# Performance work log

Measured on AMD Instinct MI355X. Metric: run time of the kernel, lower is better.

The kernel has to match this reference:

```python
import jax, jax.numpy as jnp
import numpy as np

S = 2048
D = 2048
H = 16
HD = D // H
N_CHARS = 1024
LN_EPS = 1e-5


def setup_inputs() -> dict:
    key = jax.random.key(0)
    ks = jax.random.split(key, 12)
    byte_repr = jax.random.normal(ks[0], (S, D), dtype=jnp.float32)
    categories = jax.random.randint(ks[1], (S,), 0, 32, dtype=jnp.int32)
    case = jax.random.randint(ks[2], (S,), 0, 3, dtype=jnp.int32)
    combining = jax.random.randint(ks[3], (S,), 0, 2, dtype=jnp.int32)
    seg_ids = jnp.sort(jax.random.randint(ks[4], (S,), 0, N_CHARS, dtype=jnp.int32))
    sc = 0.02
    cat_emb = jax.random.normal(ks[5], (32, D), dtype=jnp.float32) * sc
    case_emb = jax.random.normal(ks[6], (3, D), dtype=jnp.float32) * sc
    comb_emb = jax.random.normal(ks[7], (2, D), dtype=jnp.float32) * sc
    ln_g = jnp.ones((D,), dtype=jnp.float32)
    ln_b = jnp.zeros((D,), dtype=jnp.float32)
    in_w = jax.random.normal(ks[8], (3 * D, D), dtype=jnp.float32) * (1.0 / np.sqrt(D))
    in_b = jnp.zeros((3 * D,), dtype=jnp.float32)
    out_w = jax.random.normal(ks[9], (D, D), dtype=jnp.float32) * (1.0 / np.sqrt(D))
    out_b = jnp.zeros((D,), dtype=jnp.float32)
    return {
        'byte_repr': byte_repr, 'categories': categories, 'case': case,
        'combining': combining, 'seg_ids': seg_ids,
        'cat_emb': cat_emb, 'case_emb': case_emb, 'comb_emb': comb_emb,
        'ln_g': ln_g, 'ln_b': ln_b,
        'in_w': in_w, 'in_b': in_b, 'out_w': out_w, 'out_b': out_b,
    }


def reference(byte_repr, categories, case, combining, seg_ids,
              cat_emb, case_emb, comb_emb, ln_g, ln_b,
              in_w, in_b, out_w, out_b):
    # fused embedding adds
    x = byte_repr + cat_emb[categories] + case_emb[case] + comb_emb[combining]
    # LayerNorm
    mu = jnp.mean(x, axis=-1, keepdims=True)
    var = jnp.mean(jnp.square(x - mu), axis=-1, keepdims=True)
    xn = (x - mu) * jax.lax.rsqrt(var + LN_EPS) * ln_g + ln_b
    # QKV projection (torch in_proj): [S, 3D]
    qkv = xn @ in_w.T + in_b
    q, k, v = jnp.split(qkv, 3, axis=-1)
    q = q.reshape(S, H, HD).transpose(1, 0, 2)  # [H,S,hd]
    k = k.reshape(S, H, HD).transpose(1, 0, 2)
    v = v.reshape(S, H, HD).transpose(1, 0, 2)
    # additive float mask: 1 inside a character block, 0 elsewhere
    mask = (seg_ids[:, None] == seg_ids[None, :]).astype(x.dtype)
    scores = jnp.einsum('hqd,hkd->hqk', q, k) / np.sqrt(HD) + mask[None]
    attn = jax.nn.softmax(scores, axis=-1)
    o = jnp.einsum('hqk,hkd->hqd', attn, v)  # [H,S,hd]
    o = o.transpose(1, 0, 2).reshape(S, D) @ out_w.T + out_b
    # residual; dropout is identity in eval
    return xn + o
```

## Files before the change

kernel.cpp:

```cpp
#include <hip/hip_runtime.h>
#include <hip/hip_bf16.h>

#define SS 2048
#define DD 2048
#define HH 16
#define HDIM 128

typedef unsigned short u16;
typedef __attribute__((ext_vector_type(8))) short bf16x8;
typedef __attribute__((ext_vector_type(4))) float f32x4;
typedef __attribute__((ext_vector_type(16))) float f32x16;
typedef __attribute__((ext_vector_type(4))) unsigned short u16x4;
typedef __attribute__((ext_vector_type(4))) int i32x4;
typedef __attribute__((ext_vector_type(4))) unsigned int u32x4;

__device__ __forceinline__ u16 f2bf(float f){
  unsigned u = __float_as_uint(f);
  u += 0x7FFFu + ((u >> 16) & 1u);
  return (u16)(u >> 16);
}

__device__ __forceinline__ void gload_lds16(const void* g, void* l){
  __builtin_amdgcn_global_load_lds(
      (const __attribute__((address_space(1))) void*)g,
      (__attribute__((address_space(3))) void*)l, 16, 0, 0);
}

__device__ __forceinline__ f32x4 mfma16(bf16x8 a, bf16x8 b, f32x4 c){
  return __builtin_amdgcn_mfma_f32_16x16x32_bf16(a, b, c, 0, 0, 0);
}
__device__ __forceinline__ f32x16 mfma32(bf16x8 a, bf16x8 b, f32x16 c){
  return __builtin_amdgcn_mfma_f32_32x32x16_bf16(a, b, c, 0, 0, 0);
}

__global__ __launch_bounds__(256) void k_embed_ln(
    const float* __restrict__ br, const int* __restrict__ cat,
    const int* __restrict__ cse, const int* __restrict__ cmb,
    const float* __restrict__ cat_e, const float* __restrict__ case_e,
    const float* __restrict__ comb_e, const float* __restrict__ lg,
    const float* __restrict__ lb, float* __restrict__ xn32, u16* __restrict__ xn16)
{
  const int s = blockIdx.x, t = threadIdx.x;
  const int lane = t & 63, wave = t >> 6;
  const int c0 = cat[s], c1 = cse[s], c2 = cmb[s];
  const f32x4* pb = (const f32x4*)(br + (size_t)s * DD);
  const f32x4* e0 = (const f32x4*)(cat_e + (size_t)c0 * DD);
  const f32x4* e1 = (const f32x4*)(case_e + (size_t)c1 * DD);
  const f32x4* e2 = (const f32x4*)(comb_e + (size_t)c2 * DD);
  f32x4 xa = pb[t] + e0[t] + e1[t] + e2[t];
  f32x4 xb = pb[t+256] + e0[t+256] + e1[t+256] + e2[t+256];
  float s1 = 0.f, s2 = 0.f;
#pragma unroll
  for (int i = 0; i < 4; ++i){ s1 += xa[i] + xb[i]; s2 += xa[i]*xa[i] + xb[i]*xb[i]; }
#pragma unroll
  for (int off = 32; off > 0; off >>= 1){ s1 += __shfl_down(s1, off); s2 += __shfl_down(s2, off); }
  __shared__ float red[8];
  if (lane == 0){ red[wave*2] = s1; red[wave*2+1] = s2; }
  __syncthreads();
  const float t1 = red[0]+red[2]+red[4]+red[6];
  const float t2 = red[1]+red[3]+red[5]+red[7];
  const float mean = t1 * (1.0f/DD);
  const float var  = t2 * (1.0f/DD) - mean*mean;
  const float rstd = rsqrtf(var + 1e-5f);
  const f32x4* g4 = (const f32x4*)lg;
  const f32x4* b4 = (const f32x4*)lb;
  f32x4 ga = g4[t], gb = g4[t+256], ba = b4[t], bb = b4[t+256];
  f32x4 ya, yb; u16x4 ha, hb;
#pragma unroll
  for (int i = 0; i < 4; ++i){
    ya[i] = (xa[i]-mean)*rstd*ga[i] + ba[i];
    yb[i] = (xb[i]-mean)*rstd*gb[i] + bb[i];
    ha[i] = f2bf(ya[i]); hb[i] = f2bf(yb[i]);
  }
  ((f32x4*)(xn32 + (size_t)s*DD))[t]     = ya;
  ((f32x4*)(xn32 + (size_t)s*DD))[t+256] = yb;
  ((u16x4*)(xn16 + (size_t)s*DD))[t]     = ha;
  ((u16x4*)(xn16 + (size_t)s*DD))[t+256] = hb;
}

__global__ __launch_bounds__(256) void k_f32_to_bf16(
    const float* __restrict__ in, u16* __restrict__ out, int n4)
{
  int i = blockIdx.x * blockDim.x + threadIdx.x;
  const int stride = gridDim.x * blockDim.x;
  for (; i < n4; i += stride){
    f32x4 v = ((const f32x4*)in)[i];
    u16x4 h;
#pragma unroll
    for (int j = 0; j < 4; ++j) h[j] = f2bf(v[j]);
    ((u16x4*)out)[i] = h;
  }
}

__device__ __forceinline__ void gemm_tile_128(
    const u16* A, const u16* B, int K, int bm, int bn,
    u16* lds_a, u16* lds_b, f32x4 acc[4][4])
{
  const int t = threadIdx.x;
  const int lane = t & 63;
  const int wm = (t >> 6) >> 1, wn = (t >> 6) & 1;
  const int g = lane >> 4, r16 = lane & 15;
  const u16* Ab = A + (size_t)bm * 128 * K;
  const u16* Bb = B + (size_t)bn * 128 * K;
  for (int kt = 0; kt < K; kt += 32){
#pragma unroll
    for (int half = 0; half < 2; ++half){
      const int tt = half*256 + t;
      const int row = tt >> 2, col = (tt & 3) * 8;
      gload_lds16(Ab + (size_t)row*K + kt + col, lds_a + tt*8);
      gload_lds16(Bb + (size_t)row*K + kt + col, lds_b + tt*8);
    }
    __syncthreads();
    bf16x8 af[4], bfr[4];
#pragma unroll
    for (int i = 0; i < 4; ++i){
      af[i]  = *(const bf16x8*)(lds_a + (wm*64 + i*16 + r16)*32 + g*8);
      bfr[i] = *(const bf16x8*)(lds_b + (wn*64 + i*16 + r16)*32 + g*8);
    }
#pragma unroll
    for (int a = 0; a < 4; ++a)
#pragma unroll
      for (int b = 0; b < 4; ++b)
        acc[a][b] = mfma16(af[a], bfr[b], acc[a][b]);
    __syncthreads();
  }
}

__global__ __launch_bounds__(256) void k_gemm_qkv(
    const u16* __restrict__ A, const u16* __restrict__ B, const float* __restrict__ bias,
    u16* __restrict__ qws, u16* __restrict__ kws, u16* __restrict__ vtws)
{
  __shared__ __align__(16) u16 lds_a[128*32];
  __shared__ __align__(16) u16 lds_b[128*32];
  const int wg = (blockIdx.x & 7)*96 + (blockIdx.x >> 3);
  const int bm = wg & 15, bn = wg >> 4;
  f32x4 acc[4][4] = {};
  gemm_tile_128(A, B, DD, bm, bn, lds_a, lds_b, acc);
  const int t = threadIdx.x, lane = t & 63;
  const int wm = (t >> 6) >> 1, wn = (t >> 6) & 1;
  const int g = lane >> 4, r16 = lane & 15;
  const int which = bn >> 4, h = bn & 15;
  const float qscale = 0.08838834764831845f;
#pragma unroll
  for (int a = 0; a < 4; ++a){
#pragma unroll
    for (int b = 0; b < 4; ++b){
      const int hd = wn*64 + b*16 + r16;
      const float bi = bias[bn*128 + hd];
      const int s0 = bm*128 + wm*64 + a*16 + g*4;
      if (which == 0){
#pragma unroll
        for (int rr = 0; rr < 4; ++rr)
          qws[((size_t)h*SS + (s0+rr))*HDIM + hd] = f2bf((acc[a][b][rr] + bi) * qscale);
      } else if (which == 1){
#pragma unroll
        for (int rr = 0; rr < 4; ++rr)
          kws[((size_t)h*SS + (s0+rr))*HDIM + hd] = f2bf(acc[a][b][rr] + bi);
      } else {
        u16x4 pk;
#pragma unroll
        for (int rr = 0; rr < 4; ++rr) pk[rr] = f2bf(acc[a][b][rr] + bi);
        *(u16x4*)&vtws[((size_t)h*HDIM + hd)*SS + s0] = pk;
      }
    }
  }
}

__global__ __launch_bounds__(256, 2) void k_attn(
    const u16* __restrict__ q, const u16* __restrict__ kk_, const u16* __restrict__ vt,
    const int* __restrict__ seg, u16* __restrict__ o)
{
  __shared__ __align__(16) char smem[65536];
  __shared__ float stats[2][2][32];
  const int bid = blockIdx.x;
  const int xcd = bid & 7, ii = bid >> 3;
  const int h = xcd*2 + (ii >> 5), qb = ii & 31;
  const int t = threadIdx.x, lane = t & 63, w = t >> 6;
  const int hi = lane >> 5, l31 = lane & 31;
  const int p = w >> 1, qt = w & 1;
  const int q0 = qb*64 + qt*32;

  const char* khead  = (const char*)(kk_ + (size_t)h*SS*HDIM);
  const char* vthead = (const char*)(vt  + (size_t)h*HDIM*SS);

  bf16x8 qf[8];
  {
    const u16* qp = q + ((size_t)h*SS + q0 + l31)*HDIM + hi*8;
#pragma unroll
    for (int c = 0; c < 8; ++c) qf[c] = *(const bf16x8*)(qp + c*16);
  }
  const int seg_q = seg[q0 + l31];
  const int swz = l31 & 7;

  f32x16 oacc[4];
#pragma unroll
  for (int dg = 0; dg < 4; ++dg)
#pragma unroll
    for (int r = 0; r < 16; ++r) oacc[dg][r] = 0.f;
  float m = -1e30f, l = 0.f;

  auto stage = [&](int buf, int kb){
#pragma unroll
    for (int i = 0; i < 4; ++i){
      const int ci = i*256 + t;
      const int row = ci >> 4, slot = ci & 15;
      gload_lds16(khead + (size_t)(kb + row)*256 + ((slot ^ (row & 7))*16),
                  smem + buf*16384 + ci*16);
    }
#pragma unroll
    for (int i = 0; i < 4; ++i){
      const int ci = i*256 + t;
      const int row = ci >> 3, slot = ci & 7;
      gload_lds16(vthead + (size_t)row*(SS*2) + (size_t)kb*2 + ((slot ^ (row & 7))*16),
                  smem + 32768 + buf*16384 + ci*16);
    }
  };

  stage(0, 0);
  __syncthreads();

  for (int it = 0; it < 32; ++it){
    const int cur = it & 1;
    if (it < 31) stage(cur^1, (it+1)*64);

    bf16x8 kf[8];
    const char* kl = smem + cur*16384 + (p*32 + l31)*256;
#pragma unroll
    for (int c = 0; c < 8; ++c)
      kf[c] = *(const bf16x8*)(kl + (((2*c + hi) ^ swz)*16));
    const int kb_w = it*64 + p*32;
    i32x4 sg[4];
#pragma unroll
    for (int rq = 0; rq < 4; ++rq) sg[rq] = *(const i32x4*)(seg + kb_w + rq*8 + hi*4);
    bf16x8 vf[4][2];
#pragma unroll
    for (int dg = 0; dg < 4; ++dg){
      const char* vl = smem + 32768 + cur*16384 + (dg*32 + l31)*128;
#pragma unroll
      for (int ks = 0; ks < 2; ++ks)
        vf[dg][ks] = *(const bf16x8*)(vl + (((p*4 + 2*ks + hi) ^ swz)*16));
    }

    f32x16 se, so;
#pragma unroll
    for (int r = 0; r < 16; ++r){ se[r] = 0.f; so[r] = 0.f; }
#pragma unroll
    for (int c = 0; c < 4; ++c){
      se = mfma32(kf[2*c],   qf[2*c],   se);
      so = mfma32(kf[2*c+1], qf[2*c+1], so);
    }
    f32x16 s = se + so;

    float tm = -1e30f;
#pragma unroll
    for (int r = 0; r < 16; ++r){
      const int sk = sg[r>>2][r&3];
      s[r] += (sk == seg_q) ? 1.0f : 0.0f;
      tm = fmaxf(tm, s[r]);
    }
    tm = fmaxf(tm, __shfl_xor(tm, 32));
    if (!__all(tm <= m + 8.0f)){
      const float mn = fmaxf(m, tm);
      const float sc = __expf(m - mn);
      l *= sc;
#pragma unroll
      for (int dg = 0; dg < 4; ++dg)
#pragma unroll
        for (int r = 0; r < 16; ++r) oacc[dg][r] *= sc;
      m = mn;
    }
    float pr[16]; float ts = 0.f;
#pragma unroll
    for (int r = 0; r < 16; ++r){ pr[r] = __expf(s[r] - m); ts += pr[r]; }
    ts += __shfl_xor(ts, 32);
    l += ts;
    unsigned pk_[8];
#pragma unroll
    for (int i = 0; i < 8; ++i)
      pk_[i] = (unsigned)f2bf(pr[2*i]) | ((unsigned)f2bf(pr[2*i+1]) << 16);
    const unsigned x0 = __shfl_xor(hi ? pk_[0] : pk_[2], 32);
    const unsigned x1 = __shfl_xor(hi ? pk_[1] : pk_[3], 32);
    const unsigned x2 = __shfl_xor(hi ? pk_[4] : pk_[6], 32);
    const unsigned x3 = __shfl_xor(hi ? pk_[5] : pk_[7], 32);
    u32x4 f0, f1;
    f0[0] = hi ? x0 : pk_[0]; f0[1] = hi ? x1 : pk_[1];
    f0[2] = hi ? pk_[2] : x0; f0[3] = hi ? pk_[3] : x1;
    f1[0] = hi ? x2 : pk_[4]; f1[1] = hi ? x3 : pk_[5];
    f1[2] = hi ? pk_[6] : x2; f1[3] = hi ? pk_[7] : x3;
    const bf16x8 pf0 = __builtin_bit_cast(bf16x8, f0);
    const bf16x8 pf1 = __builtin_bit_cast(bf16x8, f1);
#pragma unroll
    for (int dg = 0; dg < 4; ++dg){
      oacc[dg] = mfma32(vf[dg][0], pf0, oacc[dg]);
      oacc[dg] = mfma32(vf[dg][1], pf1, oacc[dg]);
    }
    __syncthreads();
  }

  float* ob = (float*)smem;
  if (p == 1){
    if (lane < 32){ stats[qt][0][l31] = m; stats[qt][1][l31] = l; }
#pragma unroll
    for (int dg = 0; dg < 4; ++dg)
#pragma unroll
      for (int rq = 0; rq < 4; ++rq){
        f32x4 v4;
#pragma unroll
        for (int j = 0; j < 4; ++j) v4[j] = oacc[dg][rq*4 + j];
        *(f32x4*)&ob[(qt*32 + l31)*132 + dg*32 + rq*8 + hi*4] = v4;
      }
  }
  __syncthreads();
  if (p == 0){
    const float m1 = stats[qt][0][l31], l1 = stats[qt][1][l31];
    const float mM = fmaxf(m, m1);
    const float c0 = __expf(m - mM), c1 = __expf(m1 - mM);
    const float inv = 1.0f / (c0*l + c1*l1);
#pragma unroll
    for (int dg = 0; dg < 4; ++dg)
#pragma unroll
      for (int rq = 0; rq < 4; ++rq){
        const f32x4 v1 = *(const f32x4*)&ob[(qt*32 + l31)*132 + dg*32 + rq*8 + hi*4];
        u16x4 h4;
#pragma unroll
        for (int j = 0; j < 4; ++j)
          h4[j] = f2bf((c0*oacc[dg][rq*4 + j] + c1*v1[j]) * inv);
        const int d0 = dg*32 + rq*8 + hi*4;
        *(u16x4*)&o[((size_t)(q0 + l31))*DD + h*HDIM + d0] = h4;
      }
  }
}

__global__ __launch_bounds__(256) void k_gemm_out(
    const u16* __restrict__ A, const u16* __restrict__ B, const float* __restrict__ bias,
    const float* __restrict__ xn32, float* __restrict__ out)
{
  __shared__ __align__(16) u16 lds_a[128*32];
  __shared__ __align__(16) u16 lds_b[128*32];
  const int wg = (blockIdx.x & 7)*32 + (blockIdx.x >> 3);
  const int bm = wg & 15, bn = wg >> 4;
  f32x4 acc[4][4] = {};
  gemm_tile_128(A, B, DD, bm, bn, lds_a, lds_b, acc);
  const int t = threadIdx.x, lane = t & 63;
  const int wm = (t >> 6) >> 1, wn = (t >> 6) & 1;
  const int g = lane >> 4, r16 = lane & 15;
#pragma unroll
  for (int a = 0; a < 4; ++a){
#pragma unroll
    for (int b = 0; b < 4; ++b){
      const int n = bn*128 + wn*64 + b*16 + r16;
      const float bi = bias[n];
#pragma unroll
      for (int rr = 0; rr < 4; ++rr){
        const int s = bm*128 + wm*64 + a*16 + g*4 + rr;
        out[(size_t)s*DD + n] = acc[a][b][rr] + bi + xn32[(size_t)s*DD + n];
      }
    }
  }
}

extern "C" void kernel_launch(void* const* d_in, const int* in_sizes, int n_in,
                              void* d_out, int out_size, void* d_ws, size_t ws_size,
                              hipStream_t stream)
{
  (void)in_sizes; (void)n_in; (void)out_size; (void)ws_size;
  const float* br     = (const float*)d_in[0];
  const int*   cat    = (const int*)d_in[1];
  const int*   cse    = (const int*)d_in[2];
  const int*   cmb    = (const int*)d_in[3];
  const int*   seg    = (const int*)d_in[4];
  const float* cat_e  = (const float*)d_in[5];
  const float* case_e = (const float*)d_in[6];
  const float* comb_e = (const float*)d_in[7];
  const float* ln_g   = (const float*)d_in[8];
  const float* ln_b   = (const float*)d_in[9];
  const float* in_w   = (const float*)d_in[10];
  const float* in_b   = (const float*)d_in[11];
  const float* out_w  = (const float*)d_in[12];
  const float* out_b  = (const float*)d_in[13];
  float* out = (float*)d_out;

  char* ws = (char*)d_ws;
  float* xn32  = (float*)(ws);
  u16*   xn16  = (u16*)(ws + 16777216);
  u16*   inw16 = (u16*)(ws + 25165824);
  u16*   outw16= (u16*)(ws + 50331648);
  u16*   qws   = (u16*)(ws + 58720256);
  u16*   kws   = (u16*)(ws + 67108864);
  u16*   vtws  = (u16*)(ws + 75497472);
  u16*   ows   = (u16*)(ws + 83886080);

  k_embed_ln<<<SS, 256, 0, stream>>>(br, cat, cse, cmb, cat_e, case_e, comb_e,
                                     ln_g, ln_b, xn32, xn16);
  k_f32_to_bf16<<<2048, 256, 0, stream>>>(in_w, inw16, 3*DD*DD/4);
  k_f32_to_bf16<<<2048, 256, 0, stream>>>(out_w, outw16, DD*DD/4);
  k_gemm_qkv<<<768, 256, 0, stream>>>(xn16, inw16, in_b, qws, kws, vtws);
  k_attn<<<512, 256, 0, stream>>>(qws, kws, vtws, seg, ows);
  k_gemm_out<<<256, 256, 0, stream>>>(ows, outw16, out_b, xn32, out);
}
```

Measured before the change: 339.1 us.

## Rewrite QKV GEMM as 256x256 tile, 8-wave, double-buffered pipelined kernel

Replaces the 128x128 single-buffered QKV GEMM with a 256x256-tile kernel using 512 threads, BK=64, XOR-swizzled LDS and double buffering. Global-to-LDS loads for the next k-step are interleaved with four MFMA quadrants, separated by explicit barriers, vmcnt waits and setprio. The aim is to hide memory latency and raise data reuse per tile. In exchange the grid drops to 192 blocks on 256 CUs, so some CUs sit idle, and it uses 128KB of LDS per block.

```diff
diff --git a/kernel.cpp b/kernel.cpp
--- a/kernel.cpp
+++ b/kernel.cpp
@@ -32,6 +32,13 @@
 __device__ __forceinline__ f32x16 mfma32(bf16x8 a, bf16x8 b, f32x16 c){
   return __builtin_amdgcn_mfma_f32_32x32x16_bf16(a, b, c, 0, 0, 0);
 }
+
+__device__ __forceinline__ void barf(){
+  asm volatile("" ::: "memory");
+  __builtin_amdgcn_s_barrier();
+  asm volatile("" ::: "memory");
+}
+#define VMCNT2() asm volatile("s_waitcnt vmcnt(2)" ::: "memory")
 
 __global__ __launch_bounds__(256) void k_embed_ln(
     const float* __restrict__ br, const int* __restrict__ cat,
@@ -92,6 +99,151 @@
   }
 }
 
+__global__ __launch_bounds__(512) void k_gemm_qkv(
+    const u16* __restrict__ A, const u16* __restrict__ B, const float* __restrict__ bias,
+    u16* __restrict__ qws, u16* __restrict__ kws, u16* __restrict__ vtws)
+{
+  __shared__ __align__(16) u16 lds[2][4][128*64];
+  const int bid = blockIdx.x;
+  const int wg = (bid & 7)*24 + (bid >> 3);
+  const int bm = wg & 7, bn = wg >> 3;
+  const int t = threadIdx.x, lane = t & 63, wid = t >> 6;
+  const int wm = wid >> 2, wn = wid & 3;
+  const int r16 = lane & 15, g = lane >> 4;
+  const u16* Ab = A + (size_t)bm*256*DD;
+  const u16* Bb = B + (size_t)bn*256*DD;
+
+  f32x4 acc[8][4] = {};
+
+  auto stage_half = [&](int buf, int kt, int hh){
+    const u16* src = (hh < 2) ? Ab : Bb;
+    const int rbase = (hh & 1) * 128;
+    u16* dst = (u16*)&lds[buf][hh][0];
+#pragma unroll
+    for (int i = 0; i < 2; ++i){
+      const int ci = i*512 + t;
+      const int row = ci >> 3, slot = ci & 7;
+      gload_lds16(src + (size_t)(rbase + row)*DD + kt*64 + ((slot ^ (row & 7))*8),
+                  dst + ci*8);
+    }
+  };
+  auto frag = [&](const u16* half, int row, int k32) -> bf16x8 {
+    return *(const bf16x8*)((const char*)half + row*128 + (((k32*4 + g) ^ (row & 7))*16));
+  };
+
+  stage_half(0, 0, 0); stage_half(0, 0, 1); stage_half(0, 0, 2); stage_half(0, 0, 3);
+  stage_half(1, 1, 0);
+  VMCNT2();
+  barf();
+
+  const int rB0 = (wn & 1)*64 + r16;
+  for (int kt = 0; kt < 32; ++kt){
+    const int cur = kt & 1;
+    const u16* bufA = &lds[cur][wm][0];
+    const u16* bufB = &lds[cur][2 + (wn >> 1)][0];
+    bf16x8 a0[4][2], a1[4][2], b0[2][2], b1[2][2];
+#pragma unroll
+    for (int i = 0; i < 4; ++i){
+      a0[i][0] = frag(bufA, i*16 + r16, 0);
+      a0[i][1] = frag(bufA, i*16 + r16, 1);
+    }
+#pragma unroll
+    for (int j = 0; j < 2; ++j){
+      b0[j][0] = frag(bufB, rB0 + j*16, 0);
+      b0[j][1] = frag(bufB, rB0 + j*16, 1);
+    }
+    if (kt + 1 < 32) stage_half(cur^1, kt+1, 1);
+    barf();
+    __builtin_amdgcn_s_setprio(1);
+#pragma unroll
+    for (int k = 0; k < 2; ++k)
+#pragma unroll
+      for (int i = 0; i < 4; ++i)
+#pragma unroll
+        for (int j = 0; j < 2; ++j)
+          acc[i][j] = mfma16(a0[i][k], b0[j][k], acc[i][j]);
+    __builtin_amdgcn_s_setprio(0);
+    barf();
+#pragma unroll
+    for (int j = 0; j < 2; ++j){
+      b1[j][0] = frag(bufB, rB0 + (2+j)*16, 0);
+      b1[j][1] = frag(bufB, rB0 + (2+j)*16, 1);
+    }
+    if (kt + 1 < 32) stage_half(cur^1, kt+1, 2);
+    barf();
+    __builtin_amdgcn_s_setprio(1);
+#pragma unroll
+    for (int k = 0; k < 2; ++k)
+#pragma unroll
+      for (int i = 0; i < 4; ++i)
+#pragma unroll
+        for (int j = 0; j < 2; ++j)
+          acc[i][2+j] = mfma16(a0[i][k], b1[j][k], acc[i][2+j]);
+    __builtin_amdgcn_s_setprio(0);
+    barf();
+#pragma unroll
+    for (int i = 0; i < 4; ++i){
+      a1[i][0] = frag(bufA, (4+i)*16 + r16, 0);
+      a1[i][1] = frag(bufA, (4+i)*16 + r16, 1);
+    }
+    if (kt + 1 < 32) stage_half(cur^1, kt+1, 3);
+    barf();
+    __builtin_amdgcn_s_setprio(1);
+#pragma unroll
+    for (int k = 0; k < 2; ++k)
+#pragma unroll
+      for (int i = 0; i < 4; ++i)
+#pragma unroll
+        for (int j = 0; j < 2; ++j)
+          acc[4+i][2+j] = mfma16(a1[i][k], b1[j][k], acc[4+i][2+j]);
+    __builtin_amdgcn_s_setprio(0);
+    barf();
+    if (kt + 2 < 32) stage_half(cur, kt+2, 0);
+    barf();
+    __builtin_amdgcn_s_setprio(1);
+#pragma unroll
+    for (int k = 0; k < 2; ++k)
+#pragma unroll
+      for (int i = 0; i < 4; ++i)
+#pragma unroll
+        for (int j = 0; j < 2; ++j)
+          acc[4+i][j] = mfma16(a1[i][k], b0[j][k], acc[4+i][j]);
+    __builtin_amdgcn_s_setprio(0);
+    VMCNT2();
+    barf();
+  }
+
+  const float qscale = 0.08838834764831845f;
+  const int colb = bn*256 + wn*64;
+  const int rowb = bm*256 + wm*128 + g*4;
+#pragma unroll
+  for (int n = 0; n < 4; ++n){
+    const int col = colb + n*16 + r16;
+    const int which = col >> 11;
+    const int h = (col >> 7) & 15;
+    const int hd = col & 127;
+    const float bi = bias[col];
+#pragma unroll
+    for (int m = 0; m < 8; ++m){
+      const int row0 = rowb + m*16;
+      if (which == 0){
+#pragma unroll
+        for (int r = 0; r < 4; ++r)
+          qws[((size_t)h*SS + row0 + r)*HDIM + hd] = f2bf((acc[m][n][r] + bi)*qscale);
+      } else if (which == 1){
+#pragma unroll
+        for (int r = 0; r < 4; ++r)
+          kws[((size_t)h*SS + row0 + r)*HDIM + hd] = f2bf(acc[m][n][r] + bi);
+      } else {
+        u16x4 pk;
+#pragma unroll
+        for (int r = 0; r < 4; ++r) pk[r] = f2bf(acc[m][n][r] + bi);
+        *(u16x4*)&vtws[((size_t)h*HDIM + hd)*SS + row0] = pk;
+      }
+    }
+  }
+}
+
 __device__ __forceinline__ void gemm_tile_128(
     const u16* A, const u16* B, int K, int bm, int bn,
     u16* lds_a, u16* lds_b, f32x4 acc[4][4])
@@ -123,46 +275,6 @@
       for (int b = 0; b < 4; ++b)
         acc[a][b] = mfma16(af[a], bfr[b], acc[a][b]);
     __syncthreads();
-  }
-}
-
-__global__ __launch_bounds__(256) void k_gemm_qkv(
-    const u16* __restrict__ A, const u16* __restrict__ B, const float* __restrict__ bias,
-    u16* __restrict__ qws, u16* __restrict__ kws, u16* __restrict__ vtws)
-{
-  __shared__ __align__(16) u16 lds_a[128*32];
-  __shared__ __align__(16) u16 lds_b[128*32];
-  const int wg = (blockIdx.x & 7)*96 + (blockIdx.x >> 3);
-  const int bm = wg & 15, bn = wg >> 4;
-  f32x4 acc[4][4] = {};
-  gemm_tile_128(A, B, DD, bm, bn, lds_a, lds_b, acc);
-  const int t = threadIdx.x, lane = t & 63;
-  const int wm = (t >> 6) >> 1, wn = (t >> 6) & 1;
-  const int g = lane >> 4, r16 = lane & 15;
-  const int which = bn >> 4, h = bn & 15;
-  const float qscale = 0.08838834764831845f;
-#pragma unroll
-  for (int a = 0; a < 4; ++a){
-#pragma unroll
-    for (int b = 0; b < 4; ++b){
-      const int hd = wn*64 + b*16 + r16;
-      const float bi = bias[bn*128 + hd];
-      const int s0 = bm*128 + wm*64 + a*16 + g*4;
-      if (which == 0){
-#pragma unroll
-        for (int rr = 0; rr < 4; ++rr)
-          qws[((size_t)h*SS + (s0+rr))*HDIM + hd] = f2bf((acc[a][b][rr] + bi) * qscale);
-      } else if (which == 1){
-#pragma unroll
-        for (int rr = 0; rr < 4; ++rr)
-          kws[((size_t)h*SS + (s0+rr))*HDIM + hd] = f2bf(acc[a][b][rr] + bi);
-      } else {
-        u16x4 pk;
-#pragma unroll
-        for (int rr = 0; rr < 4; ++rr) pk[rr] = f2bf(acc[a][b][rr] + bi);
-        *(u16x4*)&vtws[((size_t)h*HDIM + hd)*SS + s0] = pk;
-      }
-    }
   }
 }
 
@@ -394,7 +506,7 @@
                                      ln_g, ln_b, xn32, xn16);
   k_f32_to_bf16<<<2048, 256, 0, stream>>>(in_w, inw16, 3*DD*DD/4);
   k_f32_to_bf16<<<2048, 256, 0, stream>>>(out_w, outw16, DD*DD/4);
-  k_gemm_qkv<<<768, 256, 0, stream>>>(xn16, inw16, in_b, qws, kws, vtws);
+  k_gemm_qkv<<<192, 512, 0, stream>>>(xn16, inw16, in_b, qws, kws, vtws);
   k_attn<<<512, 256, 0, stream>>>(qws, kws, vtws, seg, ows);
   k_gemm_out<<<256, 256, 0, stream>>>(ows, outw16, out_b, xn32, out);
 }
```

After: 309.6 us. 1.1x faster.
